# Kernel tuning notes

Measured on AMD Instinct MI355X. Metric: run time of the kernel, lower is better.

Reference implementation:

```python
import jax, jax.numpy as jnp
import numpy as np

B, S, H = 32, 512, 768
VOCAB, MAX_POS, TYPE_VOCAB = 30522, 512, 2
N_COLS, MAX_HLEN = 32, 16
EPS = 1e-12


def setup_inputs() -> dict:
    key = jax.random.key(0)
    ks = jax.random.split(key, 16)
    input_ids = jax.random.randint(ks[0], (B, S), 0, VOCAB)
    header_ids = jax.random.randint(ks[1], (B, N_COLS, MAX_HLEN), 0, VOCAB)
    token_type_ids = jax.random.randint(ks[2], (B, S), 0, TYPE_VOCAB)
    match_type_ids = jax.random.randint(ks[3], (B, S), 0, 11)
    type_idx = jax.random.randint(ks[4], (B, S), 0, 6)
    # distinct scatter positions per batch row (the original dict keys ki are unique)
    col_pos = jnp.sort(jnp.argsort(jax.random.uniform(ks[5], (B, S)), axis=1)[:, :N_COLS], axis=1)
    col_idx = jax.random.randint(ks[6], (B, N_COLS), 0, N_COLS)
    header_len = jax.random.randint(ks[7], (B, N_COLS), 0, MAX_HLEN + 1)  # 0 -> skip
    word_emb = jax.random.normal(ks[8], (VOCAB, H), dtype=jnp.float32) * 0.02
    pos_emb = jax.random.normal(ks[9], (MAX_POS, H), dtype=jnp.float32) * 0.02
    tok_type_emb = jax.random.normal(ks[10], (TYPE_VOCAB, H), dtype=jnp.float32) * 0.02
    match_emb = jax.random.normal(ks[11], (11, H), dtype=jnp.float32) * 0.02
    type_emb = jax.random.normal(ks[12], (6, H), dtype=jnp.float32) * 0.02
    ln_w = jnp.ones((H,), dtype=jnp.float32)
    ln_b = jnp.zeros((H,), dtype=jnp.float32)
    return {"input_ids": input_ids, "header_ids": header_ids,
            "token_type_ids": token_type_ids, "match_type_ids": match_type_ids,
            "type_idx": type_idx, "col_pos": col_pos, "col_idx": col_idx,
            "header_len": header_len, "word_emb": word_emb, "pos_emb": pos_emb,
            "tok_type_emb": tok_type_emb, "match_emb": match_emb,
            "type_emb": type_emb, "ln_w": ln_w, "ln_b": ln_b}


def reference(input_ids, header_ids, token_type_ids, match_type_ids, type_idx,
              col_pos, col_idx, header_len, word_emb, pos_emb, tok_type_emb,
              match_emb, type_emb, ln_w, ln_b):
    b, s = input_ids.shape
    words = word_emb[input_ids]                    # [B,S,H]
    header = word_emb[header_ids]                  # [B,C,L,H]
    L = header_ids.shape[2]
    # variable-length mean pool over header tokens
    mask = (jnp.arange(L)[None, None, :] < header_len[:, :, None]).astype(words.dtype)
    denom = jnp.maximum(header_len, 1).astype(words.dtype)[..., None]
    pooled = jnp.einsum('bclh,bcl->bch', header, mask) / denom   # [B,C,H]
    # scatter pooled column embeddings into word embeddings at col_pos (skip len==0)
    b_idx = jnp.arange(b)[:, None]
    sel = pooled[b_idx, col_idx]                   # [B,C,H]
    valid = (header_len[b_idx, col_idx] > 0)[..., None]
    cur = words[b_idx, col_pos]
    words = words.at[b_idx, col_pos].set(jnp.where(valid, sel, cur))
    emb = (words
           + pos_emb[jnp.arange(s)][None, :, :]
           + tok_type_emb[token_type_ids]
           + match_emb[match_type_ids]
           + type_emb[type_idx])
    # TF-style LayerNorm (eps inside sqrt)
    u = emb.mean(-1, keepdims=True)
    var = jnp.square(emb - u).mean(-1, keepdims=True)
    x = (emb - u) / jnp.sqrt(var + EPS)
    return ln_w * x + ln_b
```

## Files before the change

### kernel.cpp

```cpp
#include <hip/hip_runtime.h>

#define B_ 32
#define S_ 512
#define H_ 768
#define C_ 32
#define L_ 16

__global__ __launch_bounds__(192) void bert_emb_kernel(
    const int* __restrict__ input_ids,
    const int* __restrict__ header_ids,
    const int* __restrict__ token_type_ids,
    const int* __restrict__ match_type_ids,
    const int* __restrict__ type_idx,
    const int* __restrict__ col_pos,
    const int* __restrict__ col_idx,
    const int* __restrict__ header_len,
    const float* __restrict__ word_emb,
    const float* __restrict__ pos_emb,
    const float* __restrict__ tok_type_emb,
    const float* __restrict__ match_emb,
    const float* __restrict__ type_emb,
    const float* __restrict__ ln_w,
    const float* __restrict__ ln_b,
    float* __restrict__ out)
{
    const int bs = blockIdx.x;
    const int b  = bs >> 9;
    const int s  = bs & (S_ - 1);
    const int t  = threadIdx.x;
    const int h0 = t << 2;

    int ov = -1;
    #pragma unroll 8
    for (int c = 0; c < C_; ++c) {
        if (col_pos[b * C_ + c] == s) ov = c;
    }
    int use_pool = 0, ci = 0, hlen = 0;
    if (ov >= 0) {
        ci   = col_idx[b * C_ + ov];
        hlen = header_len[b * C_ + ci];
        if (hlen > 0) use_pool = 1;
    }

    float ax, ay, az, aw;
    if (use_pool) {
        ax = ay = az = aw = 0.f;
        const int* hid = header_ids + (b * C_ + ci) * L_;
        for (int l = 0; l < hlen; ++l) {
            float4 v = *reinterpret_cast<const float4*>(
                word_emb + (size_t)hid[l] * H_ + h0);
            ax += v.x; ay += v.y; az += v.z; aw += v.w;
        }
        float inv = 1.0f / (float)hlen;
        ax *= inv; ay *= inv; az *= inv; aw *= inv;
    } else {
        float4 v = *reinterpret_cast<const float4*>(
            word_emb + (size_t)input_ids[bs] * H_ + h0);
        ax = v.x; ay = v.y; az = v.z; aw = v.w;
    }

    {
        float4 v = *reinterpret_cast<const float4*>(pos_emb + s * H_ + h0);
        ax += v.x; ay += v.y; az += v.z; aw += v.w;
    }
    {
        float4 v = *reinterpret_cast<const float4*>(
            tok_type_emb + token_type_ids[bs] * H_ + h0);
        ax += v.x; ay += v.y; az += v.z; aw += v.w;
    }
    {
        float4 v = *reinterpret_cast<const float4*>(
            match_emb + match_type_ids[bs] * H_ + h0);
        ax += v.x; ay += v.y; az += v.z; aw += v.w;
    }
    {
        float4 v = *reinterpret_cast<const float4*>(
            type_emb + type_idx[bs] * H_ + h0);
        ax += v.x; ay += v.y; az += v.z; aw += v.w;
    }

    float s1 = ax + ay + az + aw;
    float s2 = ax * ax + ay * ay + az * az + aw * aw;
    #pragma unroll
    for (int off = 32; off > 0; off >>= 1) {
        s1 += __shfl_down(s1, off);
        s2 += __shfl_down(s2, off);
    }
    __shared__ float r1[3], r2[3];
    const int wv = t >> 6, ln = t & 63;
    if (ln == 0) { r1[wv] = s1; r2[wv] = s2; }
    __syncthreads();
    const float tot1 = r1[0] + r1[1] + r1[2];
    const float tot2 = r2[0] + r2[1] + r2[2];
    const float mean = tot1 * (1.0f / H_);
    float var = tot2 * (1.0f / H_) - mean * mean;
    var = fmaxf(var, 0.0f);
    const float rstd = rsqrtf(var + 1e-12f);

    float4 w  = *reinterpret_cast<const float4*>(ln_w + h0);
    float4 bb = *reinterpret_cast<const float4*>(ln_b + h0);
    float4 o;
    o.x = (ax - mean) * rstd * w.x + bb.x;
    o.y = (ay - mean) * rstd * w.y + bb.y;
    o.z = (az - mean) * rstd * w.z + bb.z;
    o.w = (aw - mean) * rstd * w.w + bb.w;
    *reinterpret_cast<float4*>(out + (size_t)bs * H_ + h0) = o;
}

extern "C" void kernel_launch(void* const* d_in, const int* in_sizes, int n_in,
                              void* d_out, int out_size, void* d_ws, size_t ws_size,
                              hipStream_t stream) {
    const int* input_ids      = (const int*)d_in[0];
    const int* header_ids     = (const int*)d_in[1];
    const int* token_type_ids = (const int*)d_in[2];
    const int* match_type_ids = (const int*)d_in[3];
    const int* type_idx       = (const int*)d_in[4];
    const int* col_pos        = (const int*)d_in[5];
    const int* col_idx        = (const int*)d_in[6];
    const int* header_len     = (const int*)d_in[7];
    const float* word_emb     = (const float*)d_in[8];
    const float* pos_emb      = (const float*)d_in[9];
    const float* tok_type_emb = (const float*)d_in[10];
    const float* match_emb    = (const float*)d_in[11];
    const float* type_emb     = (const float*)d_in[12];
    const float* ln_w         = (const float*)d_in[13];
    const float* ln_b         = (const float*)d_in[14];
    float* out = (float*)d_out;

    bert_emb_kernel<<<B_ * S_, 192, 0, stream>>>(
        input_ids, header_ids, token_type_ids, match_type_ids, type_idx,
        col_pos, col_idx, header_len, word_emb, pos_emb, tok_type_emb,
        match_emb, type_emb, ln_w, ln_b, out);
}
```

Before: 192.5 us.

## Assign one wavefront per token and drop shared-memory block reduction

Restructures the kernel so each 64-lane wavefront handles a whole token (three float4 chunks per lane), with four tokens per 256-thread block. The LayerNorm reduction becomes a pure xor-shuffle within the wave, removing the shared-memory exchange and __syncthreads. The serial 32-iteration col_pos scan is replaced by a ballot over lanes. This cuts per-token sync and scan overhead at the cost of more registers per thread and fewer, larger blocks.

```diff
diff --git a/kernel.cpp b/kernel.cpp
--- a/kernel.cpp
+++ b/kernel.cpp
@@ -6,7 +6,7 @@
 #define C_ 32
 #define L_ 16
 
-__global__ __launch_bounds__(192) void bert_emb_kernel(
+__global__ __launch_bounds__(256) void bert_emb_kernel(
     const int* __restrict__ input_ids,
     const int* __restrict__ header_ids,
     const int* __restrict__ token_type_ids,
@@ -24,87 +24,129 @@
     const float* __restrict__ ln_b,
     float* __restrict__ out)
 {
-    const int bs = blockIdx.x;
-    const int b  = bs >> 9;
-    const int s  = bs & (S_ - 1);
-    const int t  = threadIdx.x;
-    const int h0 = t << 2;
+    const int tok  = blockIdx.x * 4 + (threadIdx.x >> 6);
+    const int lane = threadIdx.x & 63;
+    const int b    = tok >> 9;
+    const int s    = tok & (S_ - 1);
 
-    int ov = -1;
-    #pragma unroll 8
-    for (int c = 0; c < C_; ++c) {
-        if (col_pos[b * C_ + c] == s) ov = c;
-    }
+    const int cq = lane & 31;
+    const int cp = col_pos[(b << 5) + cq];
+    unsigned long long m = __ballot(cp == s) & 0xffffffffULL;
     int use_pool = 0, ci = 0, hlen = 0;
-    if (ov >= 0) {
-        ci   = col_idx[b * C_ + ov];
-        hlen = header_len[b * C_ + ci];
-        if (hlen > 0) use_pool = 1;
+    if (m) {
+        const int cm = __ffsll((unsigned long long)m) - 1;
+        ci   = col_idx[(b << 5) + cm];
+        hlen = header_len[(b << 5) + ci];
+        use_pool = (hlen > 0);
     }
 
-    float ax, ay, az, aw;
+    const int h = lane << 2;
+    float a0x, a0y, a0z, a0w, a1x, a1y, a1z, a1w, a2x, a2y, a2z, a2w;
+
     if (use_pool) {
-        ax = ay = az = aw = 0.f;
-        const int* hid = header_ids + (b * C_ + ci) * L_;
+        a0x=a0y=a0z=a0w=a1x=a1y=a1z=a1w=a2x=a2y=a2z=a2w=0.f;
+        const int* hid = header_ids + ((b << 5) + ci) * L_;
         for (int l = 0; l < hlen; ++l) {
-            float4 v = *reinterpret_cast<const float4*>(
-                word_emb + (size_t)hid[l] * H_ + h0);
-            ax += v.x; ay += v.y; az += v.z; aw += v.w;
+            const float* r = word_emb + (size_t)hid[l] * H_ + h;
+            float4 v0 = *reinterpret_cast<const float4*>(r);
+            float4 v1 = *reinterpret_cast<const float4*>(r + 256);
+            float4 v2 = *reinterpret_cast<const float4*>(r + 512);
+            a0x+=v0.x; a0y+=v0.y; a0z+=v0.z; a0w+=v0.w;
+            a1x+=v1.x; a1y+=v1.y; a1z+=v1.z; a1w+=v1.w;
+            a2x+=v2.x; a2y+=v2.y; a2z+=v2.z; a2w+=v2.w;
         }
-        float inv = 1.0f / (float)hlen;
-        ax *= inv; ay *= inv; az *= inv; aw *= inv;
+        const float inv = 1.0f / (float)hlen;
+        a0x*=inv; a0y*=inv; a0z*=inv; a0w*=inv;
+        a1x*=inv; a1y*=inv; a1z*=inv; a1w*=inv;
+        a2x*=inv; a2y*=inv; a2z*=inv; a2w*=inv;
     } else {
-        float4 v = *reinterpret_cast<const float4*>(
-            word_emb + (size_t)input_ids[bs] * H_ + h0);
-        ax = v.x; ay = v.y; az = v.z; aw = v.w;
+        const float* r = word_emb + (size_t)input_ids[tok] * H_ + h;
+        float4 v0 = *reinterpret_cast<const float4*>(r);
+        float4 v1 = *reinterpret_cast<const float4*>(r + 256);
+        float4 v2 = *reinterpret_cast<const float4*>(r + 512);
+        a0x=v0.x; a0y=v0.y; a0z=v0.z; a0w=v0.w;
+        a1x=v1.x; a1y=v1.y; a1z=v1.z; a1w=v1.w;
+        a2x=v2.x; a2y=v2.y; a2z=v2.z; a2w=v2.w;
     }
 
     {
-        float4 v = *reinterpret_cast<const float4*>(pos_emb + s * H_ + h0);
-        ax += v.x; ay += v.y; az += v.z; aw += v.w;
+        const float* r = pos_emb + s * H_ + h;
+        float4 v0 = *reinterpret_cast<const float4*>(r);
+        float4 v1 = *reinterpret_cast<const float4*>(r + 256);
+        float4 v2 = *reinterpret_cast<const float4*>(r + 512);
+        a0x+=v0.x; a0y+=v0.y; a0z+=v0.z; a0w+=v0.w;
+        a1x+=v1.x; a1y+=v1.y; a1z+=v1.z; a1w+=v1.w;
+        a2x+=v2.x; a2y+=v2.y; a2z+=v2.z; a2w+=v2.w;
     }
     {
-        float4 v = *reinterpret_cast<const float4*>(
-            tok_type_emb + token_type_ids[bs] * H_ + h0);
-        ax += v.x; ay += v.y; az += v.z; aw += v.w;
+        const float* r = tok_type_emb + token_type_ids[tok] * H_ + h;
+        float4 v0 = *reinterpret_cast<const float4*>(r);
+        float4 v1 = *reinterpret_cast<const float4*>(r + 256);
+        float4 v2 = *reinterpret_cast<const float4*>(r + 512);
+        a0x+=v0.x; a0y+=v0.y; a0z+=v0.z; a0w+=v0.w;
+        a1x+=v1.x; a1y+=v1.y; a1z+=v1.z; a1w+=v1.w;
+        a2x+=v2.x; a2y+=v2.y; a2z+=v2.z; a2w+=v2.w;
     }
     {
-        float4 v = *reinterpret_cast<const float4*>(
-            match_emb + match_type_ids[bs] * H_ + h0);
-        ax += v.x; ay += v.y; az += v.z; aw += v.w;
+        const float* r = match_emb + match_type_ids[tok] * H_ + h;
+        float4 v0 = *reinterpret_cast<const float4*>(r);
+        float4 v1 = *reinterpret_cast<const float4*>(r + 256);
+        float4 v2 = *reinterpret_cast<const float4*>(r + 512);
+        a0x+=v0.x; a0y+=v0.y; a0z+=v0.z; a0w+=v0.w;
+        a1x+=v1.x; a1y+=v1.y; a1z+=v1.z; a1w+=v1.w;
+        a2x+=v2.x; a2y+=v2.y; a2z+=v2.z; a2w+=v2.w;
     }
     {
-        float4 v = *reinterpret_cast<const float4*>(
-            type_emb + type_idx[bs] * H_ + h0);
-        ax += v.x; ay += v.y; az += v.z; aw += v.w;
+        const float* r = type_emb + type_idx[tok] * H_ + h;
+        float4 v0 = *reinterpret_cast<const float4*>(r);
+        float4 v1 = *reinterpret_cast<const float4*>(r + 256);
+        float4 v2 = *reinterpret_cast<const float4*>(r + 512);
+        a0x+=v0.x; a0y+=v0.y; a0z+=v0.z; a0w+=v0.w;
+        a1x+=v1.x; a1y+=v1.y; a1z+=v1.z; a1w+=v1.w;
+        a2x+=v2.x; a2y+=v2.y; a2z+=v2.z; a2w+=v2.w;
     }
 
-    float s1 = ax + ay + az + aw;
-    float s2 = ax * ax + ay * ay + az * az + aw * aw;
+    float s1 = a0x+a0y+a0z+a0w + a1x+a1y+a1z+a1w + a2x+a2y+a2z+a2w;
+    float s2 = a0x*a0x+a0y*a0y+a0z*a0z+a0w*a0w
+             + a1x*a1x+a1y*a1y+a1z*a1z+a1w*a1w
+             + a2x*a2x+a2y*a2y+a2z*a2z+a2w*a2w;
     #pragma unroll
     for (int off = 32; off > 0; off >>= 1) {
-        s1 += __shfl_down(s1, off);
-        s2 += __shfl_down(s2, off);
+        s1 += __shfl_xor(s1, off);
+        s2 += __shfl_xor(s2, off);
     }
-    __shared__ float r1[3], r2[3];
-    const int wv = t >> 6, ln = t & 63;
-    if (ln == 0) { r1[wv] = s1; r2[wv] = s2; }
-    __syncthreads();
-    const float tot1 = r1[0] + r1[1] + r1[2];
-    const float tot2 = r2[0] + r2[1] + r2[2];
-    const float mean = tot1 * (1.0f / H_);
-    float var = tot2 * (1.0f / H_) - mean * mean;
+    const float mean = s1 * (1.0f / H_);
+    float var = s2 * (1.0f / H_) - mean * mean;
     var = fmaxf(var, 0.0f);
     const float rstd = rsqrtf(var + 1e-12f);
 
-    float4 w  = *reinterpret_cast<const float4*>(ln_w + h0);
-    float4 bb = *reinterpret_cast<const float4*>(ln_b + h0);
-    float4 o;
-    o.x = (ax - mean) * rstd * w.x + bb.x;
-    o.y = (ay - mean) * rstd * w.y + bb.y;
-    o.z = (az - mean) * rstd * w.z + bb.z;
-    o.w = (aw - mean) * rstd * w.w + bb.w;
-    *reinterpret_cast<float4*>(out + (size_t)bs * H_ + h0) = o;
+    const float* wp = ln_w + h;
+    const float* bp = ln_b + h;
+    float* op = out + (size_t)tok * H_ + h;
+    {
+        float4 w = *reinterpret_cast<const float4*>(wp);
+        float4 c = *reinterpret_cast<const float4*>(bp);
+        float4 o;
+        o.x=(a0x-mean)*rstd*w.x+c.x; o.y=(a0y-mean)*rstd*w.y+c.y;
+        o.z=(a0z-mean)*rstd*w.z+c.z; o.w=(a0w-mean)*rstd*w.w+c.w;
+        *reinterpret_cast<float4*>(op) = o;
+    }
+    {
+        float4 w = *reinterpret_cast<const float4*>(wp + 256);
+        float4 c = *reinterpret_cast<const float4*>(bp + 256);
+        float4 o;
+        o.x=(a1x-mean)*rstd*w.x+c.x; o.y=(a1y-mean)*rstd*w.y+c.y;
+        o.z=(a1z-mean)*rstd*w.z+c.z; o.w=(a1w-mean)*rstd*w.w+c.w;
+        *reinterpret_cast<float4*>(op + 256) = o;
+    }
+    {
+        float4 w = *reinterpret_cast<const float4*>(wp + 512);
+        float4 c = *reinterpret_cast<const float4*>(bp + 512);
+        float4 o;
+        o.x=(a2x-mean)*rstd*w.x+c.x; o.y=(a2y-mean)*rstd*w.y+c.y;
+        o.z=(a2z-mean)*rstd*w.z+c.z; o.w=(a2w-mean)*rstd*w.w+c.w;
+        *reinterpret_cast<float4*>(op + 512) = o;
+    }
 }
 
 extern "C" void kernel_launch(void* const* d_in, const int* in_sizes, int n_in,
@@ -127,7 +169,7 @@
     const float* ln_b         = (const float*)d_in[14];
     float* out = (float*)d_out;
 
-    bert_emb_kernel<<<B_ * S_, 192, 0, stream>>>(
+    bert_emb_kernel<<<(B_ * S_) / 4, 256, 0, stream>>>(
         input_ids, header_ids, token_type_ids, match_type_ids, type_idx,
         col_pos, col_idx, header_len, word_emb, pos_emb, tok_type_emb,
         match_emb, type_emb, ln_w, ln_b, out);
```

Measured after the change: 191.2 us. About the same (-0.7%).
